# Optimization experiments

Hardware: AMD Instinct MI355X
Metric: run time of the kernel (lower is better)

Reference implementation:

```python
import jax, jax.numpy as jnp
import numpy as np

DIM = 2048
NH = 16
NKV = 4
HD = DIM // NH  # 128
ROPE_BASE = 10000.0
RMS_EPS = 1.1920928955078125e-07  # torch.finfo(float32).eps, F.rms_norm default


def bitlinear(x, w, sf):
    # AnnealedBitLinear: straight-through ternary quantization
    wd = jax.lax.stop_gradient(w)
    wabs = jnp.abs(wd)
    scale = jnp.clip(jnp.mean(wabs, axis=1, keepdims=True), 1e-8)
    w_quant = jnp.sign(wd) * (wabs > 0.7 * scale).astype(w.dtype) * scale
    W = w + jax.lax.stop_gradient(sf * (w_quant - w))
    return x @ W.T


def rms_norm(x):
    return x * jax.lax.rsqrt(jnp.mean(x * x, axis=-1, keepdims=True) + RMS_EPS)


def rope_tables(seqlen, dtype):
    inv_freq = 1.0 / ROPE_BASE ** (jnp.arange(0, HD, 2, dtype=jnp.float32) / HD)
    freqs = jnp.arange(seqlen, dtype=jnp.float32)[:, None] * inv_freq[None, :]  # [T, HD/2]
    return jnp.cos(freqs).astype(dtype), jnp.sin(freqs).astype(dtype)


def apply_rotary(x, cos, sin):
    # x: [B, H, T, D]; cos/sin: [T, D/2]
    x1, x2 = x[..., : HD // 2], x[..., HD // 2 :]
    return jnp.concatenate((x1 * cos + x2 * sin, -x1 * sin + x2 * cos), axis=-1)


def setup_inputs() -> dict:
    key = jax.random.key(0)
    ks = jax.random.split(key, 6)
    B, T = 2, 2048
    bound = 1.0 / np.sqrt(DIM)  # kaiming_uniform a=sqrt(5) on [out,in]
    return {
        "x": jax.random.normal(ks[0], (B, T, DIM), dtype=jnp.float32),
        "step_fraction": jnp.float32(0.5),
        "w_q": jax.random.uniform(ks[1], (DIM, DIM), jnp.float32, -bound, bound),
        "w_k": jax.random.uniform(ks[2], (NKV * HD, DIM), jnp.float32, -bound, bound),
        "w_v": jax.random.uniform(ks[3], (NKV * HD, DIM), jnp.float32, -bound, bound),
        "w_proj": jax.random.uniform(ks[4], (DIM, DIM), jnp.float32, -bound, bound),
        "q_gain": jnp.full((NH,), 1.0, dtype=jnp.float32),
    }


def reference(x, step_fraction, w_q, w_k, w_v, w_proj, q_gain):
    B, T, _ = x.shape
    group = NH // NKV
    sf = step_fraction

    q = bitlinear(x, w_q, sf).reshape(B, T, NH, HD).transpose(0, 2, 1, 3)    # [B,NH,T,D]
    k = bitlinear(x, w_k, sf).reshape(B, T, NKV, HD).transpose(0, 2, 1, 3)  # [B,NKV,T,D]
    v = bitlinear(x, w_v, sf).reshape(B, T, NKV, HD).transpose(0, 2, 1, 3)  # [B,NKV,T,D]

    q, k = rms_norm(q), rms_norm(k)
    cos, sin = rope_tables(T, q.dtype)
    q = apply_rotary(q, cos, sin) * q_gain.astype(q.dtype)[None, :, None, None]
    k = apply_rotary(k, cos, sin)

    # GQA SDPA, causal
    qg = q.reshape(B, NKV, group, T, HD)
    scores = jnp.einsum("bhgtd,bhsd->bhgts", qg, k) / np.sqrt(HD).astype(np.float32)
    causal = jnp.tril(jnp.ones((T, T), dtype=bool))
    scores = jnp.where(causal, scores, jnp.finfo(scores.dtype).min)
    attn = jax.nn.softmax(scores, axis=-1)
    yg = jnp.einsum("bhgts,bhsd->bhgtd", attn, v)  # [B,NKV,group,T,D]

    # _xsa: per kv-head Gram-Schmidt projection of y against normalized v
    y = yg.transpose(0, 3, 1, 2, 4)                      # [B,T,NKV,group,D]
    v_bt = v.transpose(0, 2, 1, 3)                        # [B,T,NKV,D]
    vn = v_bt / jnp.maximum(jnp.linalg.norm(v_bt, axis=-1, keepdims=True), 1e-12)
    vn = vn[:, :, :, None, :]                             # [B,T,NKV,1,D]
    proj = jnp.sum(y * vn, axis=-1, keepdims=True) * vn
    y = (y - proj).reshape(B, T, NH * HD)

    return bitlinear(y, w_proj, sf)
```

## Files before the change

kernel.cpp:

```cpp
#include <hip/hip_runtime.h>

#define DIMc 2048
#define NHc 16
#define NKVc 4
#define HDc 128
#define Bc 2
#define Tc 2048
#define Mc (Bc*Tc)
#define NQKVc (DIMc + 2*NKVc*HDc)
#define TPc 2080

using f32x4 = __attribute__((ext_vector_type(4))) float;
using bf16x8 = __attribute__((ext_vector_type(8))) short;
using u16x4 = __attribute__((ext_vector_type(4))) unsigned short;
typedef unsigned short u16;

__device__ __forceinline__ float bf2f(u16 u) {
  union { unsigned int i; float f; } v; v.i = ((unsigned int)u) << 16; return v.f;
}
__device__ __forceinline__ u16 f2bf(float f) {
  union { float f; unsigned int i; } v; v.f = f;
  unsigned int r = v.i + 0x7fffu + ((v.i >> 16) & 1u);
  return (u16)(r >> 16);
}
__device__ __forceinline__ void gload_lds16(const u16* g, u16* l) {
  __builtin_amdgcn_global_load_lds((__attribute__((address_space(1))) void*)(g),
                                   (__attribute__((address_space(3))) void*)(l), 16, 0, 0);
}

__global__ __launch_bounds__(256) void prep_weights(
    const float* __restrict__ wq, const float* __restrict__ wk,
    const float* __restrict__ wv, const float* __restrict__ wp,
    const float* __restrict__ sfp,
    u16* __restrict__ Wqkv, u16* __restrict__ Wproj)
{
  int row = blockIdx.x;
  const float* src; u16* dst;
  if (row < DIMc)            { src = wq + (row)       * DIMc; dst = Wqkv + row * DIMc; }
  else if (row < DIMc + 512) { src = wk + (row-DIMc)  * DIMc; dst = Wqkv + row * DIMc; }
  else if (row < DIMc + 1024){ src = wv + (row-DIMc-512)*DIMc; dst = Wqkv + row * DIMc; }
  else                       { src = wp + (row-3072)  * DIMc; dst = Wproj + (row-3072) * DIMc; }
  int tid = threadIdx.x;
  float4 a = *(const float4*)(src + tid*8);
  float4 b = *(const float4*)(src + tid*8 + 4);
  float vals[8] = {a.x,a.y,a.z,a.w,b.x,b.y,b.z,b.w};
  float asum = 0.f;
  #pragma unroll
  for (int i = 0; i < 8; i++) asum += fabsf(vals[i]);
  #pragma unroll
  for (int mk = 1; mk < 64; mk <<= 1) asum += __shfl_xor(asum, mk);
  __shared__ float red[4];
  if ((tid & 63) == 0) red[tid >> 6] = asum;
  __syncthreads();
  float scale = fmaxf((red[0]+red[1]+red[2]+red[3]) * (1.0f/DIMc), 1e-8f);
  float thr = 0.7f * scale;
  float sfv = *sfp;
  u16 o[8];
  #pragma unroll
  for (int i = 0; i < 8; i++) {
    float w = vals[i];
    float wqv = (fabsf(w) > thr) ? (w > 0.f ? scale : -scale) : 0.f;
    o[i] = f2bf(w + sfv * (wqv - w));
  }
  *(u16x4*)(dst + tid*8)     = (u16x4){o[0],o[1],o[2],o[3]};
  *(u16x4*)(dst + tid*8 + 4) = (u16x4){o[4],o[5],o[6],o[7]};
}

__global__ __launch_bounds__(256) void cast_x(const float* __restrict__ x, u16* __restrict__ xb) {
  int i = (blockIdx.x * 256 + threadIdx.x) * 4;
  float4 v = *(const float4*)(x + i);
  *(u16x4*)(xb + i) = (u16x4){f2bf(v.x), f2bf(v.y), f2bf(v.z), f2bf(v.w)};
}

__global__ __launch_bounds__(256) void rope_table(float* __restrict__ rt) {
  int idx = blockIdx.x * 256 + threadIdx.x;
  int t = idx >> 6, j = idx & 63;
  float invf = exp2f(-(float)j * 0.207620505930460096f);
  float s, c;
  sincosf((float)t * invf, &s, &c);
  rt[idx*2]   = c;
  rt[idx*2+1] = s;
}

__global__ __launch_bounds__(256, 2) void gemm_nt(
    const u16* __restrict__ A, const u16* __restrict__ Bw,
    float* __restrict__ C, int M, int N, int K)
{
  __shared__ u16 As[128*32];
  __shared__ u16 Bs[128*32];
  const int tid = threadIdx.x;
  const int wave = tid >> 6, lane = tid & 63;
  const int bm = blockIdx.x * 128, bn = blockIdx.y * 128;

  const int srow = lane >> 2;
  const int skoff = (lane & 3) * 8;
  const u16* gA0 = A  + (bm + wave*16 + srow) * K + skoff;
  const u16* gA1 = gA0 + 64 * K;
  const u16* gB0 = Bw + (bn + wave*16 + srow) * K + skoff;
  const u16* gB1 = gB0 + 64 * K;
  u16* lA0 = &As[(wave*16) * 32];
  u16* lA1 = &As[(64 + wave*16) * 32];
  u16* lB0 = &Bs[(wave*16) * 32];
  u16* lB1 = &Bs[(64 + wave*16) * 32];

  const int wr = (wave >> 1) * 64, wc = (wave & 1) * 64;
  const int fr = lane & 15, fk = (lane >> 4) * 8;

  f32x4 acc[4][4];
  #pragma unroll
  for (int i = 0; i < 4; i++)
    #pragma unroll
    for (int j = 0; j < 4; j++) acc[i][j] = (f32x4){0.f,0.f,0.f,0.f};

  for (int k0 = 0; k0 < K; k0 += 32) {
    __syncthreads();
    gload_lds16(gA0 + k0, lA0);
    gload_lds16(gA1 + k0, lA1);
    gload_lds16(gB0 + k0, lB0);
    gload_lds16(gB1 + k0, lB1);
    __syncthreads();
    bf16x8 af[4], bfr[4];
    #pragma unroll
    for (int i = 0; i < 4; i++) {
      af[i]  = *(const bf16x8*)&As[(wr + i*16 + fr)*32 + fk];
      bfr[i] = *(const bf16x8*)&Bs[(wc + i*16 + fr)*32 + fk];
    }
    #pragma unroll
    for (int i = 0; i < 4; i++)
      #pragma unroll
      for (int j = 0; j < 4; j++)
        acc[i][j] = __builtin_amdgcn_mfma_f32_16x16x32_bf16(af[i], bfr[j], acc[i][j], 0, 0, 0);
  }
  const int col = lane & 15, rb = (lane >> 4) * 4;
  #pragma unroll
  for (int i = 0; i < 4; i++)
    #pragma unroll
    for (int j = 0; j < 4; j++) {
      int r0 = bm + wr + i*16 + rb;
      int c  = bn + wc + j*16 + col;
      #pragma unroll
      for (int r = 0; r < 4; r++)
        C[(r0 + r) * N + c] = acc[i][j][r];
    }
}

__global__ __launch_bounds__(128) void postproc(
    const float* __restrict__ qkv, const float* __restrict__ qgain,
    const float* __restrict__ rt,
    u16* __restrict__ qb, u16* __restrict__ kb, u16* __restrict__ vb)
{
  int idx = blockIdx.x;
  int slot = idx % 24;
  int m = idx / 24;
  int b = m / Tc, t = m % Tc;
  int d = threadIdx.x;
  if (slot >= 20) {
    int kvh = slot - 20;
    float val = qkv[m * NQKVc + 2560 + kvh*HDc + d];
    vb[((b*NKVc + kvh)*Tc + t)*HDc + d] = f2bf(val);
    return;
  }
  __shared__ float xn[HDc];
  __shared__ float red[2];
  bool isq = slot < 16;
  int col = isq ? slot*HDc + d : DIMc + (slot-16)*HDc + d;
  float val = qkv[m * NQKVc + col];
  float ss = val * val;
  #pragma unroll
  for (int mk = 1; mk < 64; mk <<= 1) ss += __shfl_xor(ss, mk);
  if ((d & 63) == 0) red[d >> 6] = ss;
  __syncthreads();
  float tot = red[0] + red[1];
  float rn = rsqrtf(tot * (1.0f/HDc) + 1.1920928955078125e-07f);
  xn[d] = val * rn;
  __syncthreads();
  int j = d & 63;
  float2 cs = *(const float2*)(rt + (t*64 + j)*2);
  float x1 = xn[j], x2 = xn[j + 64];
  float out = (d < 64) ? (x1*cs.x + x2*cs.y) : (-x1*cs.y + x2*cs.x);
  if (isq) {
    out *= qgain[slot];
    qb[((b*NHc + slot)*Tc + t)*HDc + d] = f2bf(out);
  } else {
    kb[((b*NKVc + (slot-16))*Tc + t)*HDc + d] = f2bf(out);
  }
}

__global__ __launch_bounds__(256) void transpose_v(
    const u16* __restrict__ vbi, u16* __restrict__ vtb)
{
  __shared__ u16 tile[64][72];
  int t0 = blockIdx.x * 64, d0 = blockIdx.y * 64, s = blockIdx.z;
  const u16* src = vbi + (size_t)s * Tc * HDc;
  u16* dst = vtb + (size_t)s * HDc * TPc;
  int tr = threadIdx.x >> 3;
  int c8 = (threadIdx.x & 7) * 8;
  #pragma unroll
  for (int i = 0; i < 2; i++) {
    int t = i*32 + tr;
    *(bf16x8*)&tile[t][c8] = *(const bf16x8*)(src + (size_t)(t0 + t)*HDc + d0 + c8);
  }
  __syncthreads();
  #pragma unroll
  for (int i = 0; i < 2; i++) {
    int d = i*32 + tr;
    u16 o[8];
    #pragma unroll
    for (int j = 0; j < 8; j++) o[j] = tile[c8 + j][d];
    *(u16x4*)(dst + (size_t)(d0 + d)*TPc + t0 + c8)     = (u16x4){o[0],o[1],o[2],o[3]};
    *(u16x4*)(dst + (size_t)(d0 + d)*TPc + t0 + c8 + 4) = (u16x4){o[4],o[5],o[6],o[7]};
  }
}

__global__ __launch_bounds__(256, 2) void attn(
    const u16* __restrict__ qb, const u16* __restrict__ kb,
    const u16* __restrict__ vtb, const u16* __restrict__ vb,
    u16* __restrict__ yb)
{
  __shared__ float Ps[4][2][16*68];

  const int tid = threadIdx.x, wave = tid >> 6, lane = tid & 63;
  const int p = blockIdx.x;
  const int bh = blockIdx.y;
  const int b = bh >> 4, h = bh & 15;
  const int kvh = h >> 2;
  const int fr = lane & 15, quad = lane >> 4;

  const int qt0 = 31 - p, qt1 = p;
  const int qw0 = qt0*64 + wave*16, qw1 = qt1*64 + wave*16;

  const u16* Qb = qb + (size_t)(b*NHc + h)*Tc*HDc;
  const u16* Kp = kb + (size_t)(b*NKVc + kvh)*Tc*HDc;
  const u16* Vp = vb + (size_t)(b*NKVc + kvh)*Tc*HDc;
  const u16* Vt = vtb + (size_t)(b*NKVc + kvh)*HDc*TPc;

  bf16x8 qf[2][4];
  #pragma unroll
  for (int c = 0; c < 4; c++) {
    qf[0][c] = *(const bf16x8*)(Qb + (size_t)(qw0 + fr)*HDc + c*32 + quad*8);
    qf[1][c] = *(const bf16x8*)(Qb + (size_t)(qw1 + fr)*HDc + c*32 + quad*8);
  }

  f32x4 Oc[2][8];
  float l_part[2][4];
  #pragma unroll
  for (int f = 0; f < 2; f++) {
    #pragma unroll
    for (int oc = 0; oc < 8; oc++) Oc[f][oc] = (f32x4){0.f,0.f,0.f,0.f};
    #pragma unroll
    for (int r = 0; r < 4; r++) l_part[f][r] = 0.f;
  }

  const float sLOG = 0.08838834764831845f * 1.4426950408889634f;
  const int ntiles = 32 - p;

  for (int it = 0; it < ntiles; it++) {
    const int kv0 = it * 64;
    const bool act1 = (it <= p);
    f32x4 s[2][4];
    #pragma unroll
    for (int cc = 0; cc < 4; cc++) { s[0][cc] = (f32x4){0.f,0.f,0.f,0.f}; s[1][cc] = (f32x4){0.f,0.f,0.f,0.f}; }
    #pragma unroll
    for (int cc = 0; cc < 4; cc++) {
      const u16* kp = Kp + (size_t)(kv0 + cc*16 + fr)*HDc + quad*8;
      bf16x8 kf0 = *(const bf16x8*)(kp);
      bf16x8 kf1 = *(const bf16x8*)(kp + 32);
      bf16x8 kf2 = *(const bf16x8*)(kp + 64);
      bf16x8 kf3 = *(const bf16x8*)(kp + 96);
      s[0][cc] = __builtin_amdgcn_mfma_f32_16x16x32_bf16(qf[0][0], kf0, s[0][cc], 0, 0, 0);
      s[0][cc] = __builtin_amdgcn_mfma_f32_16x16x32_bf16(qf[0][1], kf1, s[0][cc], 0, 0, 0);
      s[0][cc] = __builtin_amdgcn_mfma_f32_16x16x32_bf16(qf[0][2], kf2, s[0][cc], 0, 0, 0);
      s[0][cc] = __builtin_amdgcn_mfma_f32_16x16x32_bf16(qf[0][3], kf3, s[0][cc], 0, 0, 0);
      if (act1) {
        s[1][cc] = __builtin_amdgcn_mfma_f32_16x16x32_bf16(qf[1][0], kf0, s[1][cc], 0, 0, 0);
        s[1][cc] = __builtin_amdgcn_mfma_f32_16x16x32_bf16(qf[1][1], kf1, s[1][cc], 0, 0, 0);
        s[1][cc] = __builtin_amdgcn_mfma_f32_16x16x32_bf16(qf[1][2], kf2, s[1][cc], 0, 0, 0);
        s[1][cc] = __builtin_amdgcn_mfma_f32_16x16x32_bf16(qf[1][3], kf3, s[1][cc], 0, 0, 0);
      }
    }
    #pragma unroll
    for (int f = 0; f < 2; f++) {
      if (f == 0 || act1) {
        const int qtf = (f == 0) ? qt0 : qt1;
        const int qwf = (f == 0) ? qw0 : qw1;
        const bool diag = (it == qtf);
        #pragma unroll
        for (int r = 0; r < 4; r++) {
          int qrow = qwf + quad*4 + r;
          #pragma unroll
          for (int cc = 0; cc < 4; cc++) {
            float arg = s[f][cc][r] * sLOG;
            if (diag && (kv0 + cc*16 + fr > qrow)) arg = -1e30f;
            float e = exp2f(arg);
            l_part[f][r] += e;
            Ps[wave][f][(quad*4 + r)*68 + cc*16 + fr] = e;
          }
        }
      }
    }
    asm volatile("s_waitcnt lgkmcnt(0)" ::: "memory");
    bf16x8 pf[2][2];
    #pragma unroll
    for (int f = 0; f < 2; f++) {
      if (f == 0 || act1) {
        #pragma unroll
        for (int kc = 0; kc < 2; kc++) {
          f32x4 a  = *(const f32x4*)&Ps[wave][f][fr*68 + kc*32 + quad*8];
          f32x4 b2 = *(const f32x4*)&Ps[wave][f][fr*68 + kc*32 + quad*8 + 4];
          pf[f][kc] = (bf16x8){(short)f2bf(a[0]), (short)f2bf(a[1]), (short)f2bf(a[2]), (short)f2bf(a[3]),
                               (short)f2bf(b2[0]), (short)f2bf(b2[1]), (short)f2bf(b2[2]), (short)f2bf(b2[3])};
        }
      }
    }
    #pragma unroll
    for (int oc = 0; oc < 8; oc++) {
      const u16* vp = Vt + (size_t)(oc*16 + fr)*TPc + kv0 + quad*8;
      bf16x8 vf0 = *(const bf16x8*)(vp);
      bf16x8 vf1 = *(const bf16x8*)(vp + 32);
      Oc[0][oc] = __builtin_amdgcn_mfma_f32_16x16x32_bf16(pf[0][0], vf0, Oc[0][oc], 0, 0, 0);
      Oc[0][oc] = __builtin_amdgcn_mfma_f32_16x16x32_bf16(pf[0][1], vf1, Oc[0][oc], 0, 0, 0);
      if (act1) {
        Oc[1][oc] = __builtin_amdgcn_mfma_f32_16x16x32_bf16(pf[1][0], vf0, Oc[1][oc], 0, 0, 0);
        Oc[1][oc] = __builtin_amdgcn_mfma_f32_16x16x32_bf16(pf[1][1], vf1, Oc[1][oc], 0, 0, 0);
      }
    }
  }

  #pragma unroll
  for (int f = 0; f < 2; f++) {
    const int qwf = (f == 0) ? qw0 : qw1;
    #pragma unroll
    for (int r = 0; r < 4; r++) {
      int qrow = qwf + quad*4 + r;
      float l = l_part[f][r];
      l += __shfl_xor(l, 1); l += __shfl_xor(l, 2);
      l += __shfl_xor(l, 4); l += __shfl_xor(l, 8);
      float linv = 1.0f / l;
      float vv[8], dot = 0.f, n2 = 0.f;
      #pragma unroll
      for (int oc = 0; oc < 8; oc++) {
        float y = Oc[f][oc][r] * linv;
        Oc[f][oc][r] = y;
        float v = bf2f(Vp[(size_t)qrow*HDc + oc*16 + fr]);
        vv[oc] = v; dot += y * v; n2 += v * v;
      }
      dot += __shfl_xor(dot, 1); dot += __shfl_xor(dot, 2);
      dot += __shfl_xor(dot, 4); dot += __shfl_xor(dot, 8);
      n2  += __shfl_xor(n2, 1);  n2  += __shfl_xor(n2, 2);
      n2  += __shfl_xor(n2, 4);  n2  += __shfl_xor(n2, 8);
      float nn = fmaxf(sqrtf(n2), 1e-12f);
      float coef = dot / (nn * nn);
      u16* yrow = yb + ((size_t)(b*Tc) + qrow)*DIMc + h*HDc;
      #pragma unroll
      for (int oc = 0; oc < 8; oc++)
        yrow[oc*16 + fr] = f2bf(Oc[f][oc][r] - coef * vv[oc]);
    }
  }
}

extern "C" void kernel_launch(void* const* d_in, const int* in_sizes, int n_in,
                              void* d_out, int out_size, void* d_ws, size_t ws_size,
                              hipStream_t stream) {
  const float* x  = (const float*)d_in[0];
  const float* sf = (const float*)d_in[1];
  const float* wq = (const float*)d_in[2];
  const float* wk = (const float*)d_in[3];
  const float* wv = (const float*)d_in[4];
  const float* wp = (const float*)d_in[5];
  const float* qg = (const float*)d_in[6];
  float* out = (float*)d_out;

  char* p = (char*)d_ws;
  u16* Wqkv  = (u16*)p; p += (size_t)NQKVc * DIMc * 2;
  u16* Wproj = (u16*)p; p += (size_t)DIMc * DIMc * 2;
  u16* xb    = (u16*)p; p += (size_t)Mc * DIMc * 2;
  float* qkvb = (float*)p; p += (size_t)Mc * NQKVc * 4;
  u16* qbuf  = (u16*)p; p += (size_t)Bc * NHc * Tc * HDc * 2;
  u16* kbuf  = (u16*)p; p += (size_t)Bc * NKVc * Tc * HDc * 2;
  u16* vbuf  = (u16*)p; p += (size_t)Bc * NKVc * Tc * HDc * 2;
  u16* vtbuf = (u16*)p; p += (size_t)Bc * NKVc * HDc * TPc * 2;
  float* rtab = (float*)p; p += (size_t)Tc * 64 * 2 * 4;
  u16* ybuf  = xb;

  prep_weights<<<5120, 256, 0, stream>>>(wq, wk, wv, wp, sf, Wqkv, Wproj);
  cast_x<<<(Mc * DIMc) / (256 * 4), 256, 0, stream>>>(x, xb);
  rope_table<<<(Tc * 64) / 256, 256, 0, stream>>>(rtab);
  gemm_nt<<<dim3(Mc/128, NQKVc/128), 256, 0, stream>>>(xb, Wqkv, qkvb, Mc, NQKVc, DIMc);
  postproc<<<Mc * 24, 128, 0, stream>>>(qkvb, qg, rtab, qbuf, kbuf, vbuf);
  transpose_v<<<dim3(Tc/64, HDc/64, Bc*NKVc), 256, 0, stream>>>(vbuf, vtbuf);
  attn<<<dim3(16, Bc*NHc), 256, 0, stream>>>(qbuf, kbuf, vtbuf, vbuf, ybuf);
  gemm_nt<<<dim3(Mc/128, DIMc/128), 256, 0, stream>>>(ybuf, Wproj, out, Mc, DIMc, DIMc);
}
```

Before: 453.7 us.

## Split causal attention KV range in two halves and add combine kernel

Each attention block pair is split along the key/value axis into two halves, doubling the grid so more blocks run at once. Each half writes its unnormalized partial output (bf16) and row sums to a scratch buffer that reuses the no-longer-needed QKV float buffer. A new combine kernel sums the two partials, normalizes, and applies the XSA projection against normalized V. Launch bounds rise to four blocks per CU, which may force register spilling. The split also adds an extra kernel launch, extra memory traffic for the partials, and bf16 rounding of the unnormalized partials.

```diff
diff --git a/kernel.cpp b/kernel.cpp
--- a/kernel.cpp
+++ b/kernel.cpp
@@ -212,15 +212,17 @@
   }
 }
 
-__global__ __launch_bounds__(256, 2) void attn(
+__global__ __launch_bounds__(256, 4) void attn(
     const u16* __restrict__ qb, const u16* __restrict__ kb,
-    const u16* __restrict__ vtb, const u16* __restrict__ vb,
-    u16* __restrict__ yb)
+    const u16* __restrict__ vtb,
+    u16* __restrict__ Opart, float* __restrict__ lpart)
 {
   __shared__ float Ps[4][2][16*68];
 
   const int tid = threadIdx.x, wave = tid >> 6, lane = tid & 63;
-  const int p = blockIdx.x;
+  const int s_idx = blockIdx.x;
+  const int p = s_idx >> 1;
+  const int half = s_idx & 1;
   const int bh = blockIdx.y;
   const int b = bh >> 4, h = bh & 15;
   const int kvh = h >> 2;
@@ -231,7 +233,6 @@
 
   const u16* Qb = qb + (size_t)(b*NHc + h)*Tc*HDc;
   const u16* Kp = kb + (size_t)(b*NKVc + kvh)*Tc*HDc;
-  const u16* Vp = vb + (size_t)(b*NKVc + kvh)*Tc*HDc;
   const u16* Vt = vtb + (size_t)(b*NKVc + kvh)*HDc*TPc;
 
   bf16x8 qf[2][4];
@@ -252,9 +253,12 @@
   }
 
   const float sLOG = 0.08838834764831845f * 1.4426950408889634f;
-  const int ntiles = 32 - p;
-
-  for (int it = 0; it < ntiles; it++) {
+  const int niters = 32 - p;
+  const int h0end = (33 - p) >> 1;
+  const int itBeg = half ? h0end : 0;
+  const int itEnd = half ? niters : h0end;
+
+  for (int it = itBeg; it < itEnd; it++) {
     const int kv0 = it * 64;
     const bool act1 = (it <= p);
     f32x4 s[2][4];
@@ -326,6 +330,7 @@
     }
   }
 
+  const size_t hb = ((size_t)half * (Bc*NHc) + bh) * Tc;
   #pragma unroll
   for (int f = 0; f < 2; f++) {
     const int qwf = (f == 0) ? qw0 : qw1;
@@ -335,27 +340,43 @@
       float l = l_part[f][r];
       l += __shfl_xor(l, 1); l += __shfl_xor(l, 2);
       l += __shfl_xor(l, 4); l += __shfl_xor(l, 8);
-      float linv = 1.0f / l;
-      float vv[8], dot = 0.f, n2 = 0.f;
-      #pragma unroll
-      for (int oc = 0; oc < 8; oc++) {
-        float y = Oc[f][oc][r] * linv;
-        Oc[f][oc][r] = y;
-        float v = bf2f(Vp[(size_t)qrow*HDc + oc*16 + fr]);
-        vv[oc] = v; dot += y * v; n2 += v * v;
-      }
-      dot += __shfl_xor(dot, 1); dot += __shfl_xor(dot, 2);
-      dot += __shfl_xor(dot, 4); dot += __shfl_xor(dot, 8);
-      n2  += __shfl_xor(n2, 1);  n2  += __shfl_xor(n2, 2);
-      n2  += __shfl_xor(n2, 4);  n2  += __shfl_xor(n2, 8);
-      float nn = fmaxf(sqrtf(n2), 1e-12f);
-      float coef = dot / (nn * nn);
-      u16* yrow = yb + ((size_t)(b*Tc) + qrow)*DIMc + h*HDc;
+      if (fr == 0) lpart[hb + qrow] = l;
+      u16* orow = Opart + (hb + qrow) * HDc;
       #pragma unroll
       for (int oc = 0; oc < 8; oc++)
-        yrow[oc*16 + fr] = f2bf(Oc[f][oc][r] - coef * vv[oc]);
-    }
-  }
+        orow[oc*16 + fr] = f2bf(Oc[f][oc][r]);
+    }
+  }
+}
+
+__global__ __launch_bounds__(256) void combine(
+    const u16* __restrict__ Opart, const float* __restrict__ lpart,
+    const u16* __restrict__ vb, u16* __restrict__ yb)
+{
+  const int wave = threadIdx.x >> 6, lane = threadIdx.x & 63;
+  const int row = blockIdx.x * 4 + wave;
+  const int bh = row >> 11, t = row & (Tc - 1);
+  const int b = bh >> 4, h = bh & 15, kvh = h >> 2;
+  const size_t HALF = (size_t)(Bc*NHc) * Tc;
+  const size_t b0 = (size_t)row * HDc;
+  const size_t b1 = (HALF + row) * HDc;
+  float linv = 1.0f / (lpart[row] + lpart[HALF + row]);
+  const u16* vrow = vb + ((size_t)(b*NKVc + kvh)*Tc + t)*HDc;
+  float y0 = (bf2f(Opart[b0 + lane])      + bf2f(Opart[b1 + lane]))      * linv;
+  float y1 = (bf2f(Opart[b0 + 64 + lane]) + bf2f(Opart[b1 + 64 + lane])) * linv;
+  float v0 = bf2f(vrow[lane]), v1 = bf2f(vrow[64 + lane]);
+  float dot = y0*v0 + y1*v1;
+  float n2  = v0*v0 + v1*v1;
+  #pragma unroll
+  for (int mk = 1; mk < 64; mk <<= 1) {
+    dot += __shfl_xor(dot, mk);
+    n2  += __shfl_xor(n2, mk);
+  }
+  float nn = fmaxf(sqrtf(n2), 1e-12f);
+  float coef = dot / (nn * nn);
+  u16* yrow = yb + ((size_t)b*Tc + t)*DIMc + h*HDc;
+  yrow[lane]      = f2bf(y0 - coef*v0);
+  yrow[64 + lane] = f2bf(y1 - coef*v1);
 }
 
 extern "C" void kernel_launch(void* const* d_in, const int* in_sizes, int n_in,
@@ -381,6 +402,8 @@
   u16* vtbuf = (u16*)p; p += (size_t)Bc * NKVc * HDc * TPc * 2;
   float* rtab = (float*)p; p += (size_t)Tc * 64 * 2 * 4;
   u16* ybuf  = xb;
+  u16* Opart = (u16*)qkvb;
+  float* lpart = (float*)((char*)qkvb + (size_t)2 * Bc * NHc * Tc * HDc * 2);
 
   prep_weights<<<5120, 256, 0, stream>>>(wq, wk, wv, wp, sf, Wqkv, Wproj);
   cast_x<<<(Mc * DIMc) / (256 * 4), 256, 0, stream>>>(x, xb);
@@ -388,6 +411,7 @@
   gemm_nt<<<dim3(Mc/128, NQKVc/128), 256, 0, stream>>>(xb, Wqkv, qkvb, Mc, NQKVc, DIMc);
   postproc<<<Mc * 24, 128, 0, stream>>>(qkvb, qg, rtab, qbuf, kbuf, vbuf);
   transpose_v<<<dim3(Tc/64, HDc/64, Bc*NKVc), 256, 0, stream>>>(vbuf, vtbuf);
-  attn<<<dim3(16, Bc*NHc), 256, 0, stream>>>(qbuf, kbuf, vtbuf, vbuf, ybuf);
+  attn<<<dim3(32, Bc*NHc), 256, 0, stream>>>(qbuf, kbuf, vtbuf, Opart, lpart);
+  combine<<<(Bc*NHc*Tc)/4, 256, 0, stream>>>(Opart, lpart, vbuf, ybuf);
   gemm_nt<<<dim3(Mc/128, DIMc/128), 256, 0, stream>>>(ybuf, Wproj, out, Mc, DIMc, DIMc);
 }
```

New measurement: 574.7 us. 1.27x slower.
